# Optimization experiments

Hardware: AMD Instinct MI355X
Metric: run time of the kernel (lower is better)

Reference implementation:

```python
import jax, jax.numpy as jnp
import numpy as np

B, N, NB, P = 4, 2048, 10, 5
BIG = 1.0e5  # fill value for non-positive gt grasps


def _build_grasps(approach, base, contacts, thickness):
    # approach/base/contacts: [B,N,3], thickness: [B,N] -> [B,N,4,4]
    cross = jnp.cross(approach, base)
    R = jnp.stack([base, cross, approach], axis=-1)            # columns: [base, cross, approach]
    t = contacts + thickness[..., None] * 0.5 * base           # [B,N,3]
    top = jnp.concatenate([R, t[..., None]], axis=-1)          # [B,N,3,4]
    bottom = jnp.broadcast_to(jnp.array([0.0, 0.0, 0.0, 1.0], top.dtype),
                              top.shape[:-2] + (1, 4))
    return jnp.concatenate([top, bottom], axis=-2)             # [B,N,4,4]


def _transform_cps(cp_h, grasps):
    # cp_h: [P,4], grasps: [B,N,4,4] -> transformed control points [B,N,P,3]
    # torch: matmul(control_points, grasps^T)[..., :3]
    return jnp.einsum('pk,bnjk->bnpj', cp_h, grasps)[..., :3]


def _pairwise_sq(a, b):
    # a: [B,Na,P,3], b: [B,Nb,P,3] -> [B,Na,Nb] = sum_{p,c} (a-b)^2
    af = a.reshape(a.shape[0], a.shape[1], -1)
    bf = b.reshape(b.shape[0], b.shape[1], -1)
    a2 = jnp.sum(af * af, axis=-1)
    b2 = jnp.sum(bf * bf, axis=-1)
    d = a2[:, :, None] + b2[:, None, :] - 2.0 * jnp.einsum('bnd,bmd->bnm', af, bf)
    return jnp.maximum(d, 0.0)


def _forward(grasp_dir_head, approach_dir_head, grasp_offset_head, pred_points,
             binary_score_pred, binary_score_head, dir_labels_pc_cam, offset_labels_pc,
             grasp_success_labels_pc, approach_labels_pc_cam, bin_vals, bin_weights,
             control_pts, sym_control_pts):
    succ = grasp_success_labels_pc                              # [B,N] in {0,1}
    pos_in_view = jnp.maximum(jnp.sum(succ, axis=1), 1.0)       # min_geom_loss_divisor = 1.0

    # bin_offsets=True: lookup bin value of argmax bin
    thickness_pred = bin_vals[jnp.argmax(grasp_offset_head, axis=2)]   # [B,N]
    thickness_gt = bin_vals[jnp.argmax(offset_labels_pc, axis=2)]      # [B,N]

    pred_grasps = _build_grasps(approach_dir_head, grasp_dir_head, pred_points, thickness_pred)
    gt_grasps = _build_grasps(approach_labels_pc_cam, dir_labels_pc_cam, pred_points, thickness_gt)
    mask4 = succ.astype(bool)[:, :, None, None]
    pos_gt_grasps = jnp.where(mask4, gt_grasps, jnp.full_like(gt_grasps, BIG))

    ones_col = jnp.ones((P, 1), dtype=control_pts.dtype)
    cp_h = jnp.concatenate([control_pts, ones_col], axis=1)      # [P,4]
    scp_h = jnp.concatenate([sym_control_pts, ones_col], axis=1)

    pred_cp = _transform_cps(cp_h, pred_grasps)                  # [B,N,P,3]
    gt_cp_pos = _transform_cps(cp_h, pos_gt_grasps)
    sym_gt_cp_pos = _transform_cps(scp_h, pos_gt_grasps)

    # pred -> gt ADD-S (top-k with k=1 == min over concat of the two [B,N,N])
    d1 = _pairwise_sq(pred_cp, gt_cp_pos)
    d2 = _pairwise_sq(pred_cp, sym_gt_cp_pos)
    best = jnp.min(jnp.minimum(d1, d2), axis=2)                  # [B,N]
    gate = jnp.minimum(jnp.sum(succ, axis=1, keepdims=True), 1.0)
    min_adds = gate * jnp.sqrt(best)
    adds_loss = jnp.mean(binary_score_pred[:, :, 0] * min_adds)

    # gt -> pred ADD-S with unmasked gt grasps + confidence gather
    gt_cp = _transform_cps(cp_h, gt_grasps)
    sym_gt_cp = _transform_cps(scp_h, gt_grasps)
    dg1 = _pairwise_sq(gt_cp, pred_cp)                           # [B,Ngt,Npred]
    dg2 = _pairwise_sq(sym_gt_cp, pred_cp)
    m1 = jnp.min(dg1, axis=2); i1 = jnp.argmin(dg1, axis=2)
    m2 = jnp.min(dg2, axis=2); i2 = jnp.argmin(dg2, axis=2)
    # torch: where(-m1 < -m2, sym_idcs, idcs) == pick sym when m2 < m1
    idcs = jnp.where(m2 < m1, i2, i1)                            # [B,N]
    min_g2p = jnp.minimum(m1, m2) * succ
    conf = jnp.take_along_axis(binary_score_pred[:, :, 0], idcs, axis=1)
    adds_loss_gt2pred = jnp.mean(jnp.sum(conf * min_g2p, axis=1) / pos_in_view)

    # direction cosine loss
    cos_d = 1.0 - jnp.sum(dir_labels_pc_cam * grasp_dir_head, axis=2)
    dir_cosine_loss = jnp.mean(jnp.sum(cos_d * succ, axis=1) / pos_in_view)

    # approach cosine loss against orthogonalized label
    proj = jnp.sum(grasp_dir_head * approach_labels_pc_cam, axis=2, keepdims=True)
    orthog = approach_labels_pc_cam - proj * grasp_dir_head
    orthog = orthog / jnp.maximum(jnp.linalg.norm(orthog, axis=2, keepdims=True), 1e-12)
    cos_a = 1.0 - jnp.sum(orthog * approach_dir_head, axis=2)
    approach_cosine_loss = jnp.mean(jnp.sum(cos_a * succ, axis=1) / pos_in_view)

    # per-bin sigmoid BCE offset loss, bin-weighted
    bce = (offset_labels_pc * jax.nn.softplus(-grasp_offset_head)
           + (1.0 - offset_labels_pc) * jax.nn.softplus(grasp_offset_head))
    off = jnp.mean(bin_weights[None, None, :] * bce, axis=2)
    offset_loss = jnp.mean(jnp.sum(off * succ, axis=1) / pos_in_view)

    # binary success score BCE
    s = succ[:, :, None]
    score_bce = (s * jax.nn.softplus(-binary_score_head)
                 + (1.0 - s) * jax.nn.softplus(binary_score_head))
    bin_ce_loss = jnp.mean(score_bce)

    total = (1.0 * dir_cosine_loss + 1.0 * bin_ce_loss + 1.0 * offset_loss
             + 1.0 * approach_cosine_loss + 10.0 * adds_loss + 1.0 * adds_loss_gt2pred)
    return total


def setup_inputs():
    key = jax.random.key(0)
    ks = jax.random.split(key, 14)
    unit = lambda x: x / jnp.linalg.norm(x, axis=-1, keepdims=True)
    grasp_dir_head = unit(jax.random.normal(ks[0], (B, N, 3), jnp.float32))
    approach_dir_head = unit(jax.random.normal(ks[1], (B, N, 3), jnp.float32))
    grasp_offset_head = jax.random.normal(ks[2], (B, N, NB), jnp.float32)
    pred_points = jax.random.normal(ks[3], (B, N, 3), jnp.float32) * 0.3
    binary_score_pred = jax.random.uniform(ks[4], (B, N, 1), jnp.float32)
    binary_score_head = jax.random.normal(ks[5], (B, N, 1), jnp.float32)
    dir_labels_pc_cam = unit(jax.random.normal(ks[6], (B, N, 3), jnp.float32))
    offset_labels_pc = jax.nn.one_hot(jax.random.randint(ks[7], (B, N), 0, NB), NB, dtype=jnp.float32)
    grasp_success_labels_pc = jnp.round(jax.random.uniform(ks[8], (B, N), jnp.float32))
    approach_labels_pc_cam = unit(jax.random.normal(ks[9], (B, N, 3), jnp.float32))
    bin_vals = jnp.sort(jax.random.uniform(ks[10], (NB,), jnp.float32) * 0.075)
    bin_weights = jax.random.uniform(ks[11], (NB,), jnp.float32) + 0.5
    control_pts = jax.random.normal(ks[12], (P, 3), jnp.float32) * 0.05
    sym_control_pts = control_pts[jnp.array([0, 1, 3, 2, 4])]  # finger-swapped (symmetric) gripper
    return {
        'grasp_dir_head': grasp_dir_head,
        'approach_dir_head': approach_dir_head,
        'grasp_offset_head': grasp_offset_head,
        'pred_points': pred_points,
        'binary_score_pred': binary_score_pred,
        'binary_score_head': binary_score_head,
        'dir_labels_pc_cam': dir_labels_pc_cam,
        'offset_labels_pc': offset_labels_pc,
        'grasp_success_labels_pc': grasp_success_labels_pc,
        'approach_labels_pc_cam': approach_labels_pc_cam,
        'bin_vals': bin_vals,
        'bin_weights': bin_weights,
        'control_pts': control_pts,
        'sym_control_pts': sym_control_pts,
    }


def reference(grasp_dir_head, approach_dir_head, grasp_offset_head, pred_points,
              binary_score_pred, binary_score_head, dir_labels_pc_cam, offset_labels_pc,
              grasp_success_labels_pc, approach_labels_pc_cam, bin_vals, bin_weights,
              control_pts, sym_control_pts):
    return _forward(grasp_dir_head, approach_dir_head, grasp_offset_head, pred_points,
                    binary_score_pred, binary_score_head, dir_labels_pc_cam, offset_labels_pc,
                    grasp_success_labels_pc, approach_labels_pc_cam, bin_vals, bin_weights,
                    control_pts, sym_control_pts)
```

## Files before the change

kernel.cpp:

```cpp
#include <hip/hip_runtime.h>

#define Bn 4
#define Nn 2048
#define NBn 10
#define BN (Bn*Nn)
#define TCOLS 128
#define NCH 64
#define BIGM 1e32f

#define OFF_PRED 0
#define OFF_GT   (BN*16)
#define OFF_PN2  (2*BN*16)
#define OFF_GN2  (OFF_PN2 + BN)
#define OFF_BEST (OFF_GN2 + BN)
#define OFF_PK   (OFF_BEST + BN)
#define OFF_PART (OFF_PK + BN)

__device__ inline float sp_(float x) {
  return fmaxf(x, 0.0f) + log1pf(expf(-fabsf(x)));
}

__device__ inline float blockSum_(float v, float* red) {
  #pragma unroll
  for (int o = 32; o > 0; o >>= 1) v += __shfl_down(v, o, 64);
  __syncthreads();
  if ((threadIdx.x & 63) == 0) red[threadIdx.x >> 6] = v;
  __syncthreads();
  return red[0] + red[1] + red[2] + red[3];
}

__global__ __launch_bounds__(256) void k_prep(
    const float* __restrict__ gdir, const float* __restrict__ adirp,
    const float* __restrict__ goff, const float* __restrict__ ppts,
    const float* __restrict__ bsh,
    const float* __restrict__ dlab, const float* __restrict__ olab,
    const float* __restrict__ succ, const float* __restrict__ alab,
    const float* __restrict__ binv, const float* __restrict__ binw,
    const float* __restrict__ cpts, const float* __restrict__ scpts,
    float* __restrict__ ws)
{
  __shared__ float red[4];
  const int pb = blockIdx.x;
  const int idx = pb * 256 + threadIdx.x;

  const float gd0=gdir[idx*3+0],  gd1=gdir[idx*3+1],  gd2=gdir[idx*3+2];
  const float ad0=adirp[idx*3+0], ad1=adirp[idx*3+1], ad2=adirp[idx*3+2];
  const float dl0=dlab[idx*3+0],  dl1=dlab[idx*3+1],  dl2=dlab[idx*3+2];
  const float al0=alab[idx*3+0],  al1=alab[idx*3+1],  al2=alab[idx*3+2];
  const float pt0=ppts[idx*3+0],  pt1=ppts[idx*3+1],  pt2=ppts[idx*3+2];
  const float sc = succ[idx];

  float bv = goff[idx*NBn]; int ap = 0;
  #pragma unroll
  for (int k = 1; k < NBn; k++) { float v = goff[idx*NBn+k]; if (v > bv) { bv = v; ap = k; } }
  float bg = olab[idx*NBn]; int ag = 0;
  #pragma unroll
  for (int k = 1; k < NBn; k++) { float v = olab[idx*NBn+k]; if (v > bg) { bg = v; ag = k; } }
  const float tp = binv[ap] * 0.5f;
  const float tg = binv[ag] * 0.5f;

  const float cp0 = ad1*gd2 - ad2*gd1, cp1 = ad2*gd0 - ad0*gd2, cp2 = ad0*gd1 - ad1*gd0;
  const float cg0 = al1*dl2 - al2*dl1, cg1 = al2*dl0 - al0*dl2, cg2 = al0*dl1 - al1*dl0;
  const float tpx = pt0 + tp*gd0, tpy = pt1 + tp*gd1, tpz = pt2 + tp*gd2;
  const float tgx = pt0 + tg*dl0, tgy = pt1 + tg*dl1, tgz = pt2 + tg*dl2;

  float pcp[15], gcp[15];
  float pn2 = 0.f, gn2 = 0.f;
  #pragma unroll
  for (int p = 0; p < 5; p++) {
    const float cx = cpts[p*3], cy = cpts[p*3+1], cz = cpts[p*3+2];
    float x, y, z;
    x = gd0*cx + cp0*cy + ad0*cz + tpx;
    y = gd1*cx + cp1*cy + ad1*cz + tpy;
    z = gd2*cx + cp2*cy + ad2*cz + tpz;
    pcp[p*3+0]=x; pcp[p*3+1]=y; pcp[p*3+2]=z;
    pn2 = fmaf(x,x, fmaf(y,y, fmaf(z,z, pn2)));
    x = dl0*cx + cg0*cy + al0*cz + tgx;
    y = dl1*cx + cg1*cy + al1*cz + tgy;
    z = dl2*cx + cg2*cy + al2*cz + tgz;
    gcp[p*3+0]=x; gcp[p*3+1]=y; gcp[p*3+2]=z;
    gn2 = fmaf(x,x, fmaf(y,y, fmaf(z,z, gn2)));
  }

  float4* pd = (float4*)(ws + OFF_PRED) + (size_t)idx*4;
  pd[0]=make_float4(pcp[0],pcp[1],pcp[2],pcp[3]);
  pd[1]=make_float4(pcp[4],pcp[5],pcp[6],pcp[7]);
  pd[2]=make_float4(pcp[8],pcp[9],pcp[10],pcp[11]);
  pd[3]=make_float4(pcp[12],pcp[13],pcp[14],0.f);
  float4* gdst = (float4*)(ws + OFF_GT) + (size_t)idx*4;
  gdst[0]=make_float4(gcp[0],gcp[1],gcp[2],gcp[3]);
  gdst[1]=make_float4(gcp[4],gcp[5],gcp[6],gcp[7]);
  gdst[2]=make_float4(gcp[8],gcp[9],gcp[10],gcp[11]);
  gdst[3]=make_float4(gcp[12],gcp[13],gcp[14],0.f);
  ws[OFF_PN2+idx] = pn2; ws[OFF_GN2+idx] = gn2;

  ((unsigned*)ws)[OFF_BEST + idx] = 0x7F800000u;
  ((unsigned*)ws)[OFF_PK   + idx] = 0xFFFFFFFFu;

  const float cosd = 1.f - (dl0*gd0 + dl1*gd1 + dl2*gd2);
  const float proj = gd0*al0 + gd1*al1 + gd2*al2;
  const float o0 = al0 - proj*gd0, o1 = al1 - proj*gd1, o2 = al2 - proj*gd2;
  const float on = sqrtf(o0*o0 + o1*o1 + o2*o2);
  const float inv = 1.f / fmaxf(on, 1e-12f);
  const float cosa = 1.f - inv*(o0*ad0 + o1*ad1 + o2*ad2);

  float offv = 0.f;
  #pragma unroll
  for (int k = 0; k < NBn; k++) {
    const float x = goff[idx*NBn+k], lab = olab[idx*NBn+k];
    const float bce = lab * sp_(-x) + (1.f - lab) * sp_(x);
    offv = fmaf(binw[k], bce, offv);
  }
  offv *= (1.0f / NBn);
  const float sb = bsh[idx];
  const float sbce = sc * sp_(-sb) + (1.f - sc) * sp_(sb);

  float* part = ws + OFF_PART + (size_t)pb*8;
  float t;
  t = blockSum_(cosd*sc, red); if (threadIdx.x == 0) part[0] = t;
  t = blockSum_(cosa*sc, red); if (threadIdx.x == 0) part[1] = t;
  t = blockSum_(offv*sc, red); if (threadIdx.x == 0) part[2] = t;
  t = blockSum_(sc, red);      if (threadIdx.x == 0) part[3] = t;
  t = blockSum_(sbce, red);    if (threadIdx.x == 0) part[4] = t;
}

__global__ __launch_bounds__(256, 4) void k_pair(const float* __restrict__ succ,
                                                 float* __restrict__ ws) {
  __shared__ float pls[NCH*16];
  __shared__ float pn2s[NCH];
  __shared__ unsigned bkey[TCOLS];
  const int tile = blockIdx.x * TCOLS, b = blockIdx.z;
  const int bN = b * Nn;
  const int ny0 = blockIdx.y * NCH;
  const int tid = threadIdx.x;
  const int lane = tid & 63;
  const int wid = __builtin_amdgcn_readfirstlane(tid >> 6);

  {
    const int row = tid >> 2, q = tid & 3;
    ((float4*)pls)[tid] = ((const float4*)(ws + OFF_PRED))[(size_t)(bN + ny0 + row)*4 + q];
    if (tid < NCH) pn2s[tid] = ws[OFF_PN2 + bN + ny0 + tid];
    if (tid < TCOLS) bkey[tid] = 0xFFFFFFFFu;
  }

  const int r0 = bN + tile + lane;
  const int r1 = r0 + 64;
  const float4* G = (const float4*)(ws + OFF_GT);
  const float4 g00=G[(size_t)r0*4+0], g01=G[(size_t)r0*4+1], g02=G[(size_t)r0*4+2], g03=G[(size_t)r0*4+3];
  const float4 g10=G[(size_t)r1*4+0], g11=G[(size_t)r1*4+1], g12=G[(size_t)r1*4+2], g13=G[(size_t)r1*4+3];
  const float gn0 = ws[OFF_GN2+r0], gn1 = ws[OFF_GN2+r1];
  const float bias0 = (succ[r0] != 0.f) ? 0.f : BIGM;
  const float bias1 = (succ[r1] != 0.f) ? 0.f : BIGM;
  const float e0x = g02.y - g01.z, e0y = g02.z - g01.w, e0z = g02.w - g02.x;
  const float e1x = g12.y - g11.z, e1y = g12.z - g11.w, e1z = g12.w - g12.x;

  unsigned k0 = 0xFFFFFFFFu, k1 = 0xFFFFFFFFu;
  float f[16];
  __syncthreads();

  const float4* PL = (const float4*)pls + (size_t)wid*16*4;

  #pragma unroll
  for (int j = 0; j < 16; j++) {
    const float4 p0 = PL[j*4+0], p1 = PL[j*4+1], p2 = PL[j*4+2], p3 = PL[j*4+3];
    const float pn2 = pn2s[wid*16 + j];
    const float pd0 = p1.z - p2.y, pd1 = p1.w - p2.z, pd2 = p2.x - p2.w;

    float dot0, dot1, s;
    s    = fmaf(p0.w, g00.w, fmaf(p0.z, g00.z, fmaf(p0.y, g00.y, p0.x*g00.x)));
    s    = fmaf(p1.w, g01.w, fmaf(p1.z, g01.z, fmaf(p1.y, g01.y, fmaf(p1.x, g01.x, s))));
    s    = fmaf(p2.w, g02.w, fmaf(p2.z, g02.z, fmaf(p2.y, g02.y, fmaf(p2.x, g02.x, s))));
    dot0 = fmaf(p3.z, g03.z, fmaf(p3.y, g03.y, fmaf(p3.x, g03.x, s)));
    s    = fmaf(p0.w, g10.w, fmaf(p0.z, g10.z, fmaf(p0.y, g10.y, p0.x*g10.x)));
    s    = fmaf(p1.w, g11.w, fmaf(p1.z, g11.z, fmaf(p1.y, g11.y, fmaf(p1.x, g11.x, s))));
    s    = fmaf(p2.w, g12.w, fmaf(p2.z, g12.z, fmaf(p2.y, g12.y, fmaf(p2.x, g12.x, s))));
    dot1 = fmaf(p3.z, g13.z, fmaf(p3.y, g13.y, fmaf(p3.x, g13.x, s)));

    const float del0 = fmaf(pd0, e0x, fmaf(pd1, e0y, pd2*e0z));
    const float q10  = fmaf(-2.f, dot0, pn2 + gn0);
    const float d10  = fmaxf(q10, 0.f);
    const float d20  = fmaxf(fmaf(-2.f, del0, q10), 0.f);

    const float del1 = fmaf(pd0, e1x, fmaf(pd1, e1y, pd2*e1z));
    const float q11  = fmaf(-2.f, dot1, pn2 + gn1);
    const float d11  = fmaxf(q11, 0.f);
    const float d21  = fmaxf(fmaf(-2.f, del1, q11), 0.f);

    const unsigned nl = (unsigned)(ny0 + wid*16 + j), nh = nl | 0x800u;
    k0 = min(k0, min((__float_as_uint(d10) & 0xFFFFF000u) | nl,
                     (__float_as_uint(d20) & 0xFFFFF000u) | nh));
    k1 = min(k1, min((__float_as_uint(d11) & 0xFFFFF000u) | nl,
                     (__float_as_uint(d21) & 0xFFFFF000u) | nh));

    f[j] = fminf(fminf(d10, d20) + bias0, fminf(d11, d21) + bias1);
  }

  #pragma unroll
  for (int o = 1; o < 64; o <<= 1) {
    #pragma unroll
    for (int j = 0; j < 16; j++) f[j] = fminf(f[j], __shfl_xor(f[j], o, 64));
  }
  if (lane == 0) {
    #pragma unroll
    for (int j = 0; j < 16; j++)
      atomicMin((unsigned*)ws + OFF_BEST + bN + ny0 + wid*16 + j, __float_as_uint(f[j]));
  }

  atomicMin(&bkey[lane], k0);
  atomicMin(&bkey[64 + lane], k1);
  __syncthreads();
  if (tid < TCOLS)
    atomicMin((unsigned*)ws + OFF_PK + bN + tile + tid, bkey[tid]);
}

__global__ __launch_bounds__(256) void k_red(const float* __restrict__ bsp,
                                             const float* __restrict__ succ,
                                             float* __restrict__ ws) {
  __shared__ float red[4];
  const int b = blockIdx.y, nt = blockIdx.x;
  const int idx = b*Nn + nt*256 + threadIdx.x;

  const float best = __uint_as_float(((const unsigned*)ws)[OFF_BEST + idx]);
  const float adds = (best < 1e30f) ? bsp[idx] * sqrtf(best) : 0.f;

  const unsigned key = ((const unsigned*)ws)[OFF_PK + idx];
  const float d = __uint_as_float(key & 0xFFFFF000u);
  const int  id = (int)(key & 0x7FFu);
  const float g2p = bsp[b*Nn + id] * d * succ[idx];

  float* part = ws + OFF_PART + (size_t)(b*8 + nt)*8;
  float t;
  t = blockSum_(adds, red); if (threadIdx.x == 0) part[5] = t;
  t = blockSum_(g2p, red);  if (threadIdx.x == 0) part[6] = t;
}

__global__ __launch_bounds__(64) void k_fin(const float* __restrict__ ws, float* __restrict__ out) {
  const int t = threadIdx.x;
  float v[7];
  #pragma unroll
  for (int c = 0; c < 7; c++) v[c] = (t < 32) ? ws[OFF_PART + t*8 + c] : 0.f;
  #pragma unroll
  for (int o = 1; o < 8; o <<= 1) {
    #pragma unroll
    for (int c = 0; c < 7; c++) v[c] += __shfl_xor(v[c], o, 64);
  }
  const float pos = fmaxf(v[3], 1.f);
  float vb   = (v[0] + v[1] + v[2] + v[6]) / pos;
  float bce  = v[4];
  float adds = v[5];
  #pragma unroll
  for (int o = 8; o < 32; o <<= 1) {
    vb   += __shfl_xor(vb,   o, 64);
    bce  += __shfl_xor(bce,  o, 64);
    adds += __shfl_xor(adds, o, 64);
  }
  if (t == 0)
    out[0] = vb * 0.25f + bce * (1.f/BN) + 10.f * adds * (1.f/BN);
}

extern "C" void kernel_launch(void* const* d_in, const int* in_sizes, int n_in,
                              void* d_out, int out_size, void* d_ws, size_t ws_size,
                              hipStream_t stream) {
  const float* gdir  = (const float*)d_in[0];
  const float* adirp = (const float*)d_in[1];
  const float* goff  = (const float*)d_in[2];
  const float* ppts  = (const float*)d_in[3];
  const float* bsp   = (const float*)d_in[4];
  const float* bsh   = (const float*)d_in[5];
  const float* dlab  = (const float*)d_in[6];
  const float* olab  = (const float*)d_in[7];
  const float* succ  = (const float*)d_in[8];
  const float* alab  = (const float*)d_in[9];
  const float* binv  = (const float*)d_in[10];
  const float* binw  = (const float*)d_in[11];
  const float* cpts  = (const float*)d_in[12];
  const float* scpts = (const float*)d_in[13];
  float* ws  = (float*)d_ws;
  float* out = (float*)d_out;
  (void)scpts;

  k_prep<<<dim3(BN/256), dim3(256), 0, stream>>>(gdir, adirp, goff, ppts, bsh,
                                                 dlab, olab, succ, alab,
                                                 binv, binw, cpts, scpts, ws);
  k_pair<<<dim3(Nn/TCOLS, Nn/NCH, Bn), dim3(256), 0, stream>>>(succ, ws);
  k_red<<<dim3(Nn/256, Bn), dim3(256), 0, stream>>>(bsp, succ, ws);
  k_fin<<<1, 64, 0, stream>>>(ws, out);
}
```

Measured before the change: 124.6 us.

## Widen pairwise tile to 256 gt columns and use DPP wave-min reduction

```diff
diff --git a/kernel.cpp b/kernel.cpp
--- a/kernel.cpp
+++ b/kernel.cpp
@@ -4,7 +4,7 @@
 #define Nn 2048
 #define NBn 10
 #define BN (Bn*Nn)
-#define TCOLS 128
+#define TCOLS 256
 #define NCH 64
 #define BIGM 1e32f
 
@@ -18,6 +18,20 @@
 
 __device__ inline float sp_(float x) {
   return fmaxf(x, 0.0f) + log1pf(expf(-fabsf(x)));
+}
+
+__device__ inline float waveMin_(float v) {
+  const int INFI = 0x7F800000;
+#define DPPMIN(ctrl) \
+  v = fminf(v, __int_as_float(__builtin_amdgcn_update_dpp(INFI, __float_as_int(v), ctrl, 0xf, 0xf, false)))
+  DPPMIN(0x111);
+  DPPMIN(0x112);
+  DPPMIN(0x114);
+  DPPMIN(0x118);
+  DPPMIN(0x142);
+  DPPMIN(0x143);
+#undef DPPMIN
+  return v;
 }
 
 __device__ inline float blockSum_(float v, float* red) {
@@ -140,21 +154,26 @@
     const int row = tid >> 2, q = tid & 3;
     ((float4*)pls)[tid] = ((const float4*)(ws + OFF_PRED))[(size_t)(bN + ny0 + row)*4 + q];
     if (tid < NCH) pn2s[tid] = ws[OFF_PN2 + bN + ny0 + tid];
-    if (tid < TCOLS) bkey[tid] = 0xFFFFFFFFu;
-  }
-
-  const int r0 = bN + tile + lane;
-  const int r1 = r0 + 64;
+    bkey[tid] = 0xFFFFFFFFu;
+  }
+
+  float4 gq[4][4];
+  float  gnc[4], biasc[4], ex[4], ey[4], ez[4];
+  unsigned kk[4];
   const float4* G = (const float4*)(ws + OFF_GT);
-  const float4 g00=G[(size_t)r0*4+0], g01=G[(size_t)r0*4+1], g02=G[(size_t)r0*4+2], g03=G[(size_t)r0*4+3];
-  const float4 g10=G[(size_t)r1*4+0], g11=G[(size_t)r1*4+1], g12=G[(size_t)r1*4+2], g13=G[(size_t)r1*4+3];
-  const float gn0 = ws[OFF_GN2+r0], gn1 = ws[OFF_GN2+r1];
-  const float bias0 = (succ[r0] != 0.f) ? 0.f : BIGM;
-  const float bias1 = (succ[r1] != 0.f) ? 0.f : BIGM;
-  const float e0x = g02.y - g01.z, e0y = g02.z - g01.w, e0z = g02.w - g02.x;
-  const float e1x = g12.y - g11.z, e1y = g12.z - g11.w, e1z = g12.w - g12.x;
-
-  unsigned k0 = 0xFFFFFFFFu, k1 = 0xFFFFFFFFu;
+  #pragma unroll
+  for (int c = 0; c < 4; c++) {
+    const int r = bN + tile + c*64 + lane;
+    gq[c][0] = G[(size_t)r*4+0]; gq[c][1] = G[(size_t)r*4+1];
+    gq[c][2] = G[(size_t)r*4+2]; gq[c][3] = G[(size_t)r*4+3];
+    gnc[c]   = ws[OFF_GN2 + r];
+    biasc[c] = (succ[r] != 0.f) ? 0.f : BIGM;
+    ex[c] = gq[c][2].y - gq[c][1].z;
+    ey[c] = gq[c][2].z - gq[c][1].w;
+    ez[c] = gq[c][2].w - gq[c][2].x;
+    kk[c] = 0xFFFFFFFFu;
+  }
+
   float f[16];
   __syncthreads();
 
@@ -165,52 +184,41 @@
     const float4 p0 = PL[j*4+0], p1 = PL[j*4+1], p2 = PL[j*4+2], p3 = PL[j*4+3];
     const float pn2 = pn2s[wid*16 + j];
     const float pd0 = p1.z - p2.y, pd1 = p1.w - p2.z, pd2 = p2.x - p2.w;
-
-    float dot0, dot1, s;
-    s    = fmaf(p0.w, g00.w, fmaf(p0.z, g00.z, fmaf(p0.y, g00.y, p0.x*g00.x)));
-    s    = fmaf(p1.w, g01.w, fmaf(p1.z, g01.z, fmaf(p1.y, g01.y, fmaf(p1.x, g01.x, s))));
-    s    = fmaf(p2.w, g02.w, fmaf(p2.z, g02.z, fmaf(p2.y, g02.y, fmaf(p2.x, g02.x, s))));
-    dot0 = fmaf(p3.z, g03.z, fmaf(p3.y, g03.y, fmaf(p3.x, g03.x, s)));
-    s    = fmaf(p0.w, g10.w, fmaf(p0.z, g10.z, fmaf(p0.y, g10.y, p0.x*g10.x)));
-    s    = fmaf(p1.w, g11.w, fmaf(p1.z, g11.z, fmaf(p1.y, g11.y, fmaf(p1.x, g11.x, s))));
-    s    = fmaf(p2.w, g12.w, fmaf(p2.z, g12.z, fmaf(p2.y, g12.y, fmaf(p2.x, g12.x, s))));
-    dot1 = fmaf(p3.z, g13.z, fmaf(p3.y, g13.y, fmaf(p3.x, g13.x, s)));
-
-    const float del0 = fmaf(pd0, e0x, fmaf(pd1, e0y, pd2*e0z));
-    const float q10  = fmaf(-2.f, dot0, pn2 + gn0);
-    const float d10  = fmaxf(q10, 0.f);
-    const float d20  = fmaxf(fmaf(-2.f, del0, q10), 0.f);
-
-    const float del1 = fmaf(pd0, e1x, fmaf(pd1, e1y, pd2*e1z));
-    const float q11  = fmaf(-2.f, dot1, pn2 + gn1);
-    const float d11  = fmaxf(q11, 0.f);
-    const float d21  = fmaxf(fmaf(-2.f, del1, q11), 0.f);
-
     const unsigned nl = (unsigned)(ny0 + wid*16 + j), nh = nl | 0x800u;
-    k0 = min(k0, min((__float_as_uint(d10) & 0xFFFFF000u) | nl,
-                     (__float_as_uint(d20) & 0xFFFFF000u) | nh));
-    k1 = min(k1, min((__float_as_uint(d11) & 0xFFFFF000u) | nl,
-                     (__float_as_uint(d21) & 0xFFFFF000u) | nh));
-
-    f[j] = fminf(fminf(d10, d20) + bias0, fminf(d11, d21) + bias1);
-  }
-
-  #pragma unroll
-  for (int o = 1; o < 64; o <<= 1) {
+
+    float fj = BIGM * 2.f;
     #pragma unroll
-    for (int j = 0; j < 16; j++) f[j] = fminf(f[j], __shfl_xor(f[j], o, 64));
-  }
-  if (lane == 0) {
+    for (int c = 0; c < 4; c++) {
+      float s;
+      s = fmaf(p0.w, gq[c][0].w, fmaf(p0.z, gq[c][0].z, fmaf(p0.y, gq[c][0].y, p0.x*gq[c][0].x)));
+      s = fmaf(p1.w, gq[c][1].w, fmaf(p1.z, gq[c][1].z, fmaf(p1.y, gq[c][1].y, fmaf(p1.x, gq[c][1].x, s))));
+      s = fmaf(p2.w, gq[c][2].w, fmaf(p2.z, gq[c][2].z, fmaf(p2.y, gq[c][2].y, fmaf(p2.x, gq[c][2].x, s))));
+      const float dot = fmaf(p3.z, gq[c][3].z, fmaf(p3.y, gq[c][3].y, fmaf(p3.x, gq[c][3].x, s)));
+      const float del = fmaf(pd0, ex[c], fmaf(pd1, ey[c], pd2*ez[c]));
+      const float q1  = fmaf(-2.f, dot, pn2 + gnc[c]);
+      const float d1  = fmaxf(q1, 0.f);
+      const float d2  = fmaxf(fmaf(-2.f, del, q1), 0.f);
+
+      kk[c] = min(kk[c], min((__float_as_uint(d1) & 0xFFFFF000u) | nl,
+                             (__float_as_uint(d2) & 0xFFFFF000u) | nh));
+
+      fj = fminf(fj, fminf(d1, d2) + biasc[c]);
+    }
+    f[j] = fj;
+  }
+
+  #pragma unroll
+  for (int j = 0; j < 16; j++) f[j] = waveMin_(f[j]);
+  if (lane == 63) {
     #pragma unroll
     for (int j = 0; j < 16; j++)
       atomicMin((unsigned*)ws + OFF_BEST + bN + ny0 + wid*16 + j, __float_as_uint(f[j]));
   }
 
-  atomicMin(&bkey[lane], k0);
-  atomicMin(&bkey[64 + lane], k1);
-  __syncthreads();
-  if (tid < TCOLS)
-    atomicMin((unsigned*)ws + OFF_PK + bN + tile + tid, bkey[tid]);
+  #pragma unroll
+  for (int c = 0; c < 4; c++) atomicMin(&bkey[c*64 + lane], kk[c]);
+  __syncthreads();
+  atomicMin((unsigned*)ws + OFF_PK + bN + tile + tid, bkey[tid]);
 }
 
 __global__ __launch_bounds__(256) void k_red(const float* __restrict__ bsp,
```

Result: slower. 141.2 us (+13.3%).
